# Performance work log

Measured on AMD Instinct MI355X. Metric: run time of the kernel, lower is better.

The kernel has to match this reference:

```python
import jax, jax.numpy as jnp
import numpy as np

B, L, K, H = 256, 256, 128, 256


def setup_inputs() -> dict:
    key = jax.random.key(0)
    ks = jax.random.split(key, 24)

    def u(k, shape, fan):
        s = 1.0 / np.sqrt(fan)
        return jax.random.uniform(k, shape, minval=-s, maxval=s, dtype=jnp.float32)

    x = jax.random.normal(ks[0], (B, L, K), jnp.float32)
    mask = (jax.random.uniform(ks[1], (B, L, K)) < 0.7).astype(jnp.float32)
    record_num = jax.random.randint(ks[2], (B,), L // 2, L + 1)
    ts = jnp.cumsum(jax.random.uniform(ks[3], (B, L), minval=0.1, maxval=1.0, dtype=jnp.float32), axis=1)
    time_stamp = ts * (jnp.arange(L)[None, :] < record_num[:, None]).astype(jnp.float32)

    return {
        "x": x,
        "mask": mask,
        "time_stamp": time_stamp,
        # TemporalDecay h: W [H,K], stdv = 1/sqrt(out)=1/sqrt(H)
        "W_gh": u(ks[4], (H, K), H), "b_gh": u(ks[5], (H,), H),
        # TemporalDecay x (diag): W [K,K], stdv = 1/sqrt(K)
        "W_gx": u(ks[6], (K, K), K), "b_gx": u(ks[7], (K,), K),
        # hist_reg: Linear(H -> K), stdv = 1/sqrt(H)
        "W_hist": u(ks[8], (K, H), H), "b_hist": u(ks[9], (K,), H),
        "W_feat": u(ks[10], (K, K), K), "b_feat": u(ks[11], (K,), K),
        # weight_combine: Linear(2K -> K), stdv = 1/sqrt(2K)
        "W_comb": u(ks[12], (K, 2 * K), 2 * K), "b_comb": u(ks[13], (K,), 2 * K),
        # GRUCell(2K -> H): uniform 1/sqrt(H)
        "W_ih": u(ks[14], (3 * H, 2 * K), H), "W_hh": u(ks[15], (3 * H, H), H),
        "b_ih": u(ks[16], (3 * H,), H), "b_hh": u(ks[17], (3 * H,), H),
        # out: Linear(H -> 1)
        "W_out": u(ks[18], (1, H), H), "b_out": u(ks[19], (1,), H),
        "record_num": record_num,
        "direct": 0,
    }


def _forward(x, mask, time_stamp, W_gh, b_gh, W_gx, b_gx, W_hist, b_hist,
             W_feat, b_feat, W_comb, b_comb, W_ih, W_hh, b_ih, b_hh,
             W_out, b_out, record_num):
    Bs, Ls, Ks = x.shape
    Hs = W_gh.shape[0]
    eye = jnp.eye(Ks, dtype=x.dtype)
    W_gx_m = W_gx * eye                 # diag temporal decay
    W_feat_m = W_feat * (1.0 - eye)

    # --- deltas (gen_aux_data): d[0]=1; d[t] = |ts[t]-ts[t-1]| + (1-m[t])*d[t-1] ---
    gaps = jnp.abs(jnp.diff(time_stamp, axis=1))          # [B, L-1]
    mask_t = jnp.swapaxes(mask, 0, 1)                     # [L, B, K]

    def dstep(prev, inp):
        gap, m = inp                                      # [B], [B,K]
        d = gap[:, None] + (1.0 - m) * prev
        return d, d

    d0 = jnp.ones((Bs, Ks), x.dtype)
    _, drest = jax.lax.scan(dstep, d0, (gaps.T, mask_t[1:]))
    deltas = jnp.concatenate([d0[None], drest], axis=0)   # [L, B, K]
    valid = (jnp.arange(Ls)[:, None] < record_num[None, :])  # break at record_num
    deltas = jnp.where(valid[:, :, None], deltas, 0.0)

    evals = (time_stamp != 0).astype(x.dtype)             # [B, L]

    x_t = jnp.swapaxes(x, 0, 1)                           # [L, B, K]
    e_t = evals.T                                         # [L, B]

    def step(carry, inp):
        h, xloss = carry
        xt, mt, dt, et = inp                              # [B,K],[B,K],[B,K],[B]
        e_m = et[:, None]
        gamma_h = jnp.exp(-jax.nn.relu(dt @ W_gh.T + b_gh))   # [B,H]
        gamma_x = jnp.exp(-jax.nn.relu(dt @ W_gx_m.T + b_gx)) # [B,K]
        h_prev = h
        h = h * gamma_h
        x_h = h @ W_hist.T + b_hist
        msum = jnp.sum(mt) + 1e-5
        xloss = xloss + jnp.sum(jnp.abs(xt - x_h) * mt) / msum
        x_c = mt * xt + (1.0 - mt) * x_h
        z_h = x_c @ W_feat_m.T + b_feat
        xloss = xloss + jnp.sum(jnp.abs(xt - z_h) * mt * e_m) / msum
        alpha = jnp.concatenate([gamma_x, mt], axis=1) @ W_comb.T + b_comb
        c_h = alpha * z_h + (1.0 - alpha) * x_h
        xloss = xloss + jnp.sum(jnp.abs(xt - c_h) * mt * e_m) / msum
        c_c = mt * xt + (1.0 - mt) * c_h
        inputs = jnp.concatenate([c_c, mt], axis=1)           # [B, 2K]
        gi = inputs @ W_ih.T + b_ih                           # [B, 3H]
        gh = h @ W_hh.T + b_hh
        ir, iz, ig = jnp.split(gi, 3, axis=1)
        hr, hz, hg = jnp.split(gh, 3, axis=1)
        r = jax.nn.sigmoid(ir + hr)
        z = jax.nn.sigmoid(iz + hz)
        n = jnp.tanh(ig + r * hg)
        h_new = (1.0 - z) * n + z * h
        h_new = h_new * e_m + (1.0 - e_m) * h_prev            # freeze h past record
        return (h_new, xloss), c_c * e_m

    h0 = jnp.zeros((Bs, Hs), x.dtype)
    (h_fin, x_loss), imps = jax.lax.scan(step, (h0, jnp.float32(0.0)), (x_t, mask_t, deltas, e_t))
    imputations = jnp.swapaxes(imps, 0, 1)                # [B, L, K]
    predictions = jax.nn.sigmoid(h_fin @ W_out.T + b_out) # [B, 1]
    return imputations, x_loss, predictions


def reference(x, mask, time_stamp, W_gh, b_gh, W_gx, b_gx, W_hist, b_hist,
              W_feat, b_feat, W_comb, b_comb, W_ih, W_hh, b_ih, b_hh,
              W_out, b_out, record_num, direct):
    return _forward(x, mask, time_stamp, W_gh, b_gh, W_gx, b_gx, W_hist, b_hist,
                    W_feat, b_feat, W_comb, b_comb, W_ih, W_hh, b_ih, b_hh,
                    W_out, b_out, record_num)
```

## Files before the change

kernel.cpp:

```cpp
#include <hip/hip_runtime.h>
#include <math.h>

#define BT 256
#define LT 256
#define KT 128
#define HT 256
#define LOSS_IDX ((size_t)BT*LT*KT)
#define PRED_IDX (LOSS_IDX + 1)
#define LDP 1280
#define GH0 0
#define AL0 256
#define GI0 384
#define ZP0 1152

typedef _Float16 h2 __attribute__((ext_vector_type(2)));
typedef _Float16 f16x8 __attribute__((ext_vector_type(8)));
typedef float f32x4 __attribute__((ext_vector_type(4)));

__device__ __forceinline__ float fd2(h2 a, h2 b, float c){
#if __has_builtin(__builtin_amdgcn_fdot2)
  return __builtin_amdgcn_fdot2(a, b, c, false);
#else
  return c + (float)a[0]*(float)b[0] + (float)a[1]*(float)b[1];
#endif
}
__device__ __forceinline__ float dot8(f16x8 w, f16x8 a, float acc){
  acc = fd2(__builtin_shufflevector(w,w,0,1), __builtin_shufflevector(a,a,0,1), acc);
  acc = fd2(__builtin_shufflevector(w,w,2,3), __builtin_shufflevector(a,a,2,3), acc);
  acc = fd2(__builtin_shufflevector(w,w,4,5), __builtin_shufflevector(a,a,4,5), acc);
  acc = fd2(__builtin_shufflevector(w,w,6,7), __builtin_shufflevector(a,a,6,7), acc);
  return acc;
}
__device__ __forceinline__ float sigf(float v){ return 1.0f/(1.0f + __expf(-v)); }
__device__ __forceinline__ float tanh_fast(float v){
  float a = fminf(fabsf(v), 15.0f);
  float e2 = __expf(2.0f*a);
  float r = (e2 - 1.0f)/(e2 + 1.0f);
  return copysignf(r, v);
}
__device__ __forceinline__ float f16bits(unsigned u, int hi){
  union { unsigned short s; _Float16 h; } c;
  c.s = (unsigned short)(hi ? (u >> 16) : (u & 0xffff));
  return (float)c.h;
}

__global__ void pack_cast(const float* __restrict__ src, _Float16* __restrict__ dst,
                          int J, int Kd, int diag, int total){
  int idx = blockIdx.x*256 + threadIdx.x;
  if (idx >= total) return;
  float v = src[idx];
  if (diag && (idx / Kd) == (idx % Kd)) v = 0.0f;
  dst[idx] = (_Float16)v;
}
__global__ void pack_rowchunks(const float* __restrict__ src, _Float16* __restrict__ dst,
                               int J, int K, int total){
  int idx = blockIdx.x*256 + threadIdx.x;
  if (idx >= total) return;
  int j = idx % J, c = idx / J;
  #pragma unroll
  for (int e = 0; e < 8; ++e)
    dst[(size_t)idx*8 + e] = (_Float16)src[(size_t)j*K + c*8 + e];
}
__global__ void pack_col(const float* __restrict__ src, _Float16* __restrict__ dst,
                         int J, int Kc, int ld, int diag, int total){
  int idx = blockIdx.x*256 + threadIdx.x;
  if (idx >= total) return;
  int j = idx % J, k = idx / J;
  float v = src[(size_t)j*ld + k];
  if (diag && j == k) v = 0.0f;
  dst[idx] = (_Float16)v;
}

__global__ __launch_bounds__(128) void scan_kernel(
    const float* __restrict__ x, const float* __restrict__ mask, const float* __restrict__ ts,
    const float* __restrict__ W_gx, const float* __restrict__ b_gx,
    const int* __restrict__ record_num,
    _Float16* __restrict__ deltas, _Float16* __restrict__ Agx, _Float16* __restrict__ U)
{
  int b = blockIdx.x, k = threadIdx.x;
  int rn = record_num[b];
  float gxd = W_gx[(size_t)k*KT + k];
  float bgx = b_gx[k];
  float d = 1.0f, tsp = 0.0f;
  for (int t0 = 0; t0 < LT; t0 += 8){
    float xv[8], mv[8], tsv[8];
    #pragma unroll
    for (int u = 0; u < 8; ++u){
      size_t off = ((size_t)b*LT + t0 + u)*KT + k;
      xv[u] = x[off]; mv[u] = mask[off];
      tsv[u] = ts[(size_t)b*LT + t0 + u];
    }
    #pragma unroll
    for (int u = 0; u < 8; ++u){
      int t = t0 + u;
      if (t > 0){
        float gap = fabsf(tsv[u] - (u ? tsv[u-1] : tsp));
        d = gap + (1.0f - mv[u])*d;
      }
      float e = (t < rn) ? 1.0f : 0.0f;
      float dev = d * e;
      size_t row = (size_t)b*LT + t;
      deltas[row*KT + k] = (_Float16)dev;
      float gx = __expf(-fmaxf(fmaf(dev, gxd, bgx), 0.0f));
      Agx[row*2*KT + k]      = (_Float16)gx;
      Agx[row*2*KT + KT + k] = (_Float16)mv[u];
      U[row*2*KT + k]        = (_Float16)(mv[u]*xv[u]);
      U[row*2*KT + KT + k]   = (_Float16)mv[u];
    }
    tsp = tsv[7];
  }
}

__global__ void msum_kernel(const float* __restrict__ mask, float* __restrict__ msumInv){
  __shared__ float red[256];
  int t = blockIdx.x;
  float acc = 0.0f;
  for (int i = threadIdx.x; i < BT*KT; i += 256){
    int b = i >> 7, k = i & 127;
    acc += mask[((size_t)b*LT + t)*KT + k];
  }
  red[threadIdx.x] = acc; __syncthreads();
  for (int s = 128; s > 0; s >>= 1){
    if (threadIdx.x < s) red[threadIdx.x] += red[threadIdx.x + s];
    __syncthreads();
  }
  if (threadIdx.x == 0) msumInv[t] = 1.0f/(red[0] + 1e-5f);
}

__global__ __launch_bounds__(256) void gemm_f16(
    const _Float16* __restrict__ A, long ldA, int K,
    const _Float16* __restrict__ B, long ldB,
    _Float16* __restrict__ C, long colofs,
    const float* __restrict__ bias, int op)
{
  const int w = threadIdx.x >> 6, lane = threadIdx.x & 63;
  const int ml = lane & 15, quad = lane >> 4;
  const long m0 = (long)blockIdx.x*64 + w*16;
  const long nb0 = (long)blockIdx.y*64;
  f32x4 acc[4] = {{0,0,0,0},{0,0,0,0},{0,0,0,0},{0,0,0,0}};
  for (int kc = 0; kc < K; kc += 32){
    f16x8 a = *(const f16x8*)(A + (m0 + ml)*ldA + kc + quad*8);
    #pragma unroll
    for (int nt = 0; nt < 4; ++nt){
      f16x8 bfr = *(const f16x8*)(B + (nb0 + nt*16 + ml)*ldB + kc + quad*8);
      acc[nt] = __builtin_amdgcn_mfma_f32_16x16x32_f16(a, bfr, acc[nt], 0, 0, 0);
    }
  }
  #pragma unroll
  for (int nt = 0; nt < 4; ++nt){
    long col = nb0 + nt*16 + ml;
    float bv = (op >= 1) ? bias[col] : 0.0f;
    #pragma unroll
    for (int r = 0; r < 4; ++r){
      float v = acc[nt][r];
      if (op >= 1) v += bv;
      if (op == 2) v = __expf(-fmaxf(v, 0.0f));
      long row = m0 + quad*4 + r;
      C[row*LDP + colofs + col] = (_Float16)v;
    }
  }
}

#define NT 768

struct __align__(16) SeqS {
  f16x8 whist_l[32*128];
  _Float16 wfc_l[128*128];
  float h[HT];
  float hs[HT];
  alignas(16) _Float16 hsh[HT];
  float gh[3*HT];
  float gi[3*HT];
  float xh[KT];
  float part6[6][KT];
  float v3[KT], v5[KT];
  int lidx[136];
  int posk[KT];
  int cnt;
  unsigned pb[2][LDP/2];
  float xb[2][KT], mb[2][KT];
  float bhist[KT], bfeat[KT];
  float bhh[3*HT];
  float wout[HT];
  float minv[LT];
  float red[NT/64];
};

__global__ __launch_bounds__(NT, 1) void rits_seq(
    const float* __restrict__ x, const float* __restrict__ mask,
    const int* __restrict__ record_num, const float* __restrict__ msumInv,
    const _Float16* __restrict__ P,
    const f16x8* __restrict__ Whh_p, const f16x8* __restrict__ Whist_p,
    const _Float16* __restrict__ Wfc, const _Float16* __restrict__ Wihc,
    const float* __restrict__ b_hist, const float* __restrict__ b_feat,
    const float* __restrict__ b_hh,
    const float* __restrict__ W_out, const float* __restrict__ b_out,
    float* __restrict__ out)
{
  __shared__ SeqS s;
  const int tid = threadIdx.x;
  const int b = blockIdx.x;
  const int rn = record_num[b];
  const unsigned* __restrict__ Pd = (const unsigned*)P + (size_t)b*LT*(LDP/2);

  for (int i = tid; i < 32*128; i += NT) s.whist_l[i] = Whist_p[i];
  for (int i = tid; i < 128*128/2; i += NT)
    ((unsigned*)s.wfc_l)[i] = ((const unsigned*)Wfc)[i];
  if (tid < HT) s.h[tid] = 0.0f;
  if (tid < KT){ s.bhist[tid] = b_hist[tid]; s.bfeat[tid] = b_feat[tid]; }
  if (tid < 3*HT) s.bhh[tid] = b_hh[tid];
  if (tid < 136) s.lidx[tid] = 0;
  if (tid >= 256 && tid < 512) s.wout[tid - 256] = W_out[tid - 256];
  if (tid >= 512 && tid < 512 + LT) s.minv[tid - 512] = msumInv[tid - 512];
  if (tid < LDP/2) s.pb[0][tid] = Pd[tid];
  else if (tid < LDP/2 + KT){
    int k = tid - LDP/2;
    s.xb[0][k] = x[((size_t)b*LT)*KT + k];
    s.mb[0][k] = mask[((size_t)b*LT)*KT + k];
  }
  __syncthreads();

  float loss = 0.0f;

  for (int t = 0; t < LT; ++t){
    const int cur = t & 1, nxt = cur ^ 1;

    unsigned pr0 = 0; float prx = 0.0f, prm = 0.0f;
    if (t < LT - 1){
      if (tid < LDP/2) pr0 = Pd[(size_t)(t+1)*(LDP/2) + tid];
      else {
        int k = tid - LDP/2;
        size_t offx = ((size_t)b*LT + t + 1)*KT + k;
        prx = x[offx]; prm = mask[offx];
      }
    }
    if (tid == 0) s.cnt = 0;
    if (tid < HT){
      float g = f16bits(s.pb[cur][tid >> 1], tid & 1);
      float hsv = s.h[tid] * g;
      s.hs[tid] = hsv;
      s.hsh[tid] = (_Float16)hsv;
    }
    __syncthreads();

    {
      const f16x8* hp = (const f16x8*)s.hsh;
      if (tid < KT){
        float a2 = 0.0f;
        #pragma unroll 8
        for (int c = 0; c < 32; ++c)
          a2 = dot8(s.whist_l[c*128 + tid], hp[c], a2);
        float xh = a2 + s.bhist[tid];
        s.xh[tid] = xh;
        float mv = s.mb[cur][tid], xv = s.xb[cur][tid];
        loss += fabsf(xv - xh) * mv * s.minv[t];
        if (mv == 0.0f){
          int pp = atomicAdd(&s.cnt, 1);
          s.lidx[pp] = tid; s.v3[pp] = xh; s.posk[tid] = pp;
        }
      }
      float acc = 0.0f;
      #pragma unroll 8
      for (int c = 0; c < 32; ++c)
        acc = dot8(Whh_p[c*768 + tid], hp[c], acc);
      s.gh[tid] = acc;
    }
    __syncthreads();

    const int c0 = s.cnt;
    const int c4 = (c0 + 7) & ~7;
    {
      int st = tid >> 7, j = tid & 127;
      float a = 0.0f;
      for (int i = st; i < c0; i += 6)
        a += s.v3[i] * (float)s.wfc_l[s.lidx[i]*128 + j];
      s.part6[st][j] = a;
    }
    float wpre[16];
    #pragma unroll
    for (int u = 0; u < 16; ++u)
      wpre[u] = (u < c4) ? (float)Wihc[(size_t)s.lidx[u]*768 + tid] : 0.0f;
    __syncthreads();

    if (tid < KT){
      const int j = tid;
      if (j >= c0 && j < c4) s.v5[j] = 0.0f;
      float z = f16bits(s.pb[cur][ZP0/2 + (j >> 1)], j & 1) + s.bfeat[j]
              + s.part6[0][j] + s.part6[1][j] + s.part6[2][j]
              + s.part6[3][j] + s.part6[4][j] + s.part6[5][j];
      float al = f16bits(s.pb[cur][AL0/2 + (j >> 1)], j & 1);
      float xh = s.xh[j];
      float mv = s.mb[cur][j], xv = s.xb[cur][j];
      float e = (t < rn) ? 1.0f : 0.0f;
      float inv = s.minv[t];
      float ch = al*z + (1.0f - al)*xh;
      loss += (fabsf(xv - z) + fabsf(xv - ch)) * mv * e * inv;
      float cc = mv*xv + (1.0f - mv)*ch;
      out[((size_t)b*LT + t)*KT + j] = cc * e;
      if (mv == 0.0f) s.v5[s.posk[j]] = ch;
    }
    __syncthreads();

    {
      float g = f16bits(s.pb[cur][GI0/2 + (tid >> 1)], tid & 1);
      #pragma unroll
      for (int u = 0; u < 16; ++u)
        if (u < c4) g += s.v5[u] * wpre[u];
      for (int i = 16; i < c4; i += 8){
        #pragma unroll
        for (int u = 0; u < 8; ++u)
          g += s.v5[i + u] * (float)Wihc[(size_t)s.lidx[i + u]*768 + tid];
      }
      s.gi[tid] = g;
    }
    __syncthreads();

    if (tid < HT){
      const int j = tid;
      float ir = s.gi[j], iz = s.gi[HT + j], ig = s.gi[2*HT + j];
      float hr = s.gh[j] + s.bhh[j];
      float hz = s.gh[HT + j] + s.bhh[HT + j];
      float hg = s.gh[2*HT + j] + s.bhh[2*HT + j];
      float r = sigf(ir + hr);
      float zg = sigf(iz + hz);
      float n = tanh_fast(ig + r*hg);
      float hn = (1.0f - zg)*n + zg*s.hs[j];
      if (t < rn) s.h[j] = hn;
    }
    if (t < LT - 1){
      if (tid < LDP/2) s.pb[nxt][tid] = pr0;
      else {
        int k = tid - LDP/2;
        s.xb[nxt][k] = prx; s.mb[nxt][k] = prm;
      }
    }
    __syncthreads();
  }

  #pragma unroll
  for (int off = 32; off; off >>= 1) loss += __shfl_down(loss, off);
  if ((tid & 63) == 0) s.red[tid >> 6] = loss;
  __syncthreads();
  if (tid == 0){
    float tot = 0.0f;
    #pragma unroll
    for (int w = 0; w < NT/64; ++w) tot += s.red[w];
    atomicAdd(&out[LOSS_IDX], tot);
  }

  if (tid < HT) s.gh[tid] = s.h[tid] * s.wout[tid];
  __syncthreads();
  for (int st2 = 128; st2 > 0; st2 >>= 1){
    if (tid < st2) s.gh[tid] += s.gh[tid + st2];
    __syncthreads();
  }
  if (tid == 0) out[PRED_IDX + b] = sigf(s.gh[0] + b_out[0]);
}

extern "C" void kernel_launch(void* const* d_in, const int* in_sizes, int n_in,
                              void* d_out, int out_size, void* d_ws, size_t ws_size,
                              hipStream_t stream){
  const float* x      = (const float*)d_in[0];
  const float* mask   = (const float*)d_in[1];
  const float* ts     = (const float*)d_in[2];
  const float* W_gh   = (const float*)d_in[3];
  const float* b_gh   = (const float*)d_in[4];
  const float* W_gx   = (const float*)d_in[5];
  const float* b_gx   = (const float*)d_in[6];
  const float* W_hist = (const float*)d_in[7];
  const float* b_hist = (const float*)d_in[8];
  const float* W_feat = (const float*)d_in[9];
  const float* b_feat = (const float*)d_in[10];
  const float* W_comb = (const float*)d_in[11];
  const float* b_comb = (const float*)d_in[12];
  const float* W_ih   = (const float*)d_in[13];
  const float* W_hh   = (const float*)d_in[14];
  const float* b_ih   = (const float*)d_in[15];
  const float* b_hh   = (const float*)d_in[16];
  const float* W_out  = (const float*)d_in[17];
  const float* b_out  = (const float*)d_in[18];
  const int*   rn     = (const int*)d_in[19];
  float* out = (float*)d_out;
  char* ws = (char*)d_ws;

  size_t off = 0;
  auto alloc = [&](size_t bytes) -> char* {
    char* p = ws + off;
    off += (bytes + 255) & ~(size_t)255;
    return p;
  };
  _Float16* P      = (_Float16*)alloc((size_t)BT*LT*LDP*2);
  _Float16* deltas = (_Float16*)alloc((size_t)BT*LT*KT*2);
  _Float16* Agx    = (_Float16*)alloc((size_t)BT*LT*2*KT*2);
  _Float16* U      = (_Float16*)alloc((size_t)BT*LT*2*KT*2);
  _Float16* WghF   = (_Float16*)alloc(HT*KT*2);
  _Float16* WcombF = (_Float16*)alloc(KT*2*KT*2);
  _Float16* WihF   = (_Float16*)alloc(3*HT*2*KT*2);
  _Float16* WfeatF = (_Float16*)alloc(KT*KT*2);
  _Float16* Whh_p  = (_Float16*)alloc(3*HT*HT*2);
  _Float16* Whist_p= (_Float16*)alloc(KT*HT*2);
  _Float16* Wfc    = (_Float16*)alloc(KT*KT*2);
  _Float16* Wihc   = (_Float16*)alloc(KT*3*HT*2);
  float* msumInv   = (float*)alloc(LT*4);

  auto grid1 = [](int n){ return dim3((n + 255)/256); };
  pack_cast<<<grid1(HT*KT), 256, 0, stream>>>(W_gh, WghF, HT, KT, 0, HT*KT);
  pack_cast<<<grid1(KT*2*KT), 256, 0, stream>>>(W_comb, WcombF, KT, 2*KT, 0, KT*2*KT);
  pack_cast<<<grid1(3*HT*2*KT), 256, 0, stream>>>(W_ih, WihF, 3*HT, 2*KT, 0, 3*HT*2*KT);
  pack_cast<<<grid1(KT*KT), 256, 0, stream>>>(W_feat, WfeatF, KT, KT, 1, KT*KT);
  pack_rowchunks<<<grid1(3*HT*(HT/8)), 256, 0, stream>>>(W_hh, Whh_p, 3*HT, HT, 3*HT*(HT/8));
  pack_rowchunks<<<grid1(KT*(HT/8)), 256, 0, stream>>>(W_hist, Whist_p, KT, HT, KT*(HT/8));
  pack_col<<<grid1(KT*KT), 256, 0, stream>>>(W_feat, Wfc, KT, KT, KT, 1, KT*KT);
  pack_col<<<grid1(768*KT), 256, 0, stream>>>(W_ih, Wihc, 3*HT, KT, 2*KT, 0, 3*HT*KT);

  scan_kernel<<<dim3(BT), dim3(KT), 0, stream>>>(x, mask, ts, W_gx, b_gx, rn, deltas, Agx, U);
  msum_kernel<<<dim3(LT), dim3(256), 0, stream>>>(mask, msumInv);

  const int MR = BT*LT;
  gemm_f16<<<dim3(MR/64, HT/64), 256, 0, stream>>>(deltas, KT, KT, WghF, KT, P, GH0, b_gh, 2);
  gemm_f16<<<dim3(MR/64, KT/64), 256, 0, stream>>>(Agx, 2*KT, 2*KT, WcombF, 2*KT, P, AL0, b_comb, 1);
  gemm_f16<<<dim3(MR/64, 3*HT/64), 256, 0, stream>>>(U, 2*KT, 2*KT, WihF, 2*KT, P, GI0, b_ih, 1);
  gemm_f16<<<dim3(MR/64, KT/64), 256, 0, stream>>>(U, 2*KT, KT, WfeatF, KT, P, ZP0, (const float*)nullptr, 0);

  hipMemsetAsync((void*)(out + LOSS_IDX), 0, sizeof(float), stream);

  rits_seq<<<dim3(BT), dim3(NT), 0, stream>>>(x, mask, rn, msumInv, P,
      (const f16x8*)Whh_p, (const f16x8*)Whist_p, Wfc, Wihc,
      b_hist, b_feat, b_hh, W_out, b_out, out);
}
```

Baseline: 2.420 ms.

## Restructure recurrent step with warp specialization and fewer barriers per timestep

Raises the block to 1024 threads and gives each warp group a role: W_hh matvec, hist regression with ballot-based compaction of missing features, or prefetch of the next step's precomputed data. The decayed-hidden computation for the next step is folded into the GRU update, and the feature-regression partial-sum stage is merged into the combine stage. Together these remove two barriers per timestep. Dot products now use four independent fdot2 accumulators, and the sparse W_ih gather uses packed fp16 pairs. The cost is fewer threads doing the serial z accumulation, fp16 rounding of the imputed values, and higher register pressure at 1024 threads.

```diff
diff --git a/kernel.cpp b/kernel.cpp
--- a/kernel.cpp
+++ b/kernel.cpp
@@ -24,13 +24,10 @@
   return c + (float)a[0]*(float)b[0] + (float)a[1]*(float)b[1];
 #endif
 }
-__device__ __forceinline__ float dot8(f16x8 w, f16x8 a, float acc){
-  acc = fd2(__builtin_shufflevector(w,w,0,1), __builtin_shufflevector(a,a,0,1), acc);
-  acc = fd2(__builtin_shufflevector(w,w,2,3), __builtin_shufflevector(a,a,2,3), acc);
-  acc = fd2(__builtin_shufflevector(w,w,4,5), __builtin_shufflevector(a,a,4,5), acc);
-  acc = fd2(__builtin_shufflevector(w,w,6,7), __builtin_shufflevector(a,a,6,7), acc);
-  return acc;
-}
+__device__ __forceinline__ h2 lo2(f16x8 v){ return __builtin_shufflevector(v,v,0,1); }
+__device__ __forceinline__ h2 p1(f16x8 v){ return __builtin_shufflevector(v,v,2,3); }
+__device__ __forceinline__ h2 p2(f16x8 v){ return __builtin_shufflevector(v,v,4,5); }
+__device__ __forceinline__ h2 p3(f16x8 v){ return __builtin_shufflevector(v,v,6,7); }
 __device__ __forceinline__ float sigf(float v){ return 1.0f/(1.0f + __expf(-v)); }
 __device__ __forceinline__ float tanh_fast(float v){
   float a = fminf(fabsf(v), 15.0f);
@@ -161,7 +158,7 @@
   }
 }
 
-#define NT 768
+#define NT 1024
 
 struct __align__(16) SeqS {
   f16x8 whist_l[32*128];
@@ -172,12 +169,13 @@
   float gh[3*HT];
   float gi[3*HT];
   float xh[KT];
-  float part6[6][KT];
-  float v3[KT], v5[KT];
+  float v3[136];
+  alignas(4) _Float16 v5h[136];
   int lidx[136];
   int posk[KT];
   int cnt;
-  unsigned pb[2][LDP/2];
+  unsigned gam[2][128];
+  unsigned pbd[2][512];
   float xb[2][KT], mb[2][KT];
   float bhist[KT], bfeat[KT];
   float bhh[3*HT];
@@ -206,89 +204,105 @@
   for (int i = tid; i < 32*128; i += NT) s.whist_l[i] = Whist_p[i];
   for (int i = tid; i < 128*128/2; i += NT)
     ((unsigned*)s.wfc_l)[i] = ((const unsigned*)Wfc)[i];
-  if (tid < HT) s.h[tid] = 0.0f;
+  if (tid < HT){ s.h[tid] = 0.0f; s.hs[tid] = 0.0f; s.hsh[tid] = (_Float16)0.0f; }
   if (tid < KT){ s.bhist[tid] = b_hist[tid]; s.bfeat[tid] = b_feat[tid]; }
   if (tid < 3*HT) s.bhh[tid] = b_hh[tid];
   if (tid < 136) s.lidx[tid] = 0;
-  if (tid >= 256 && tid < 512) s.wout[tid - 256] = W_out[tid - 256];
+  if (tid >= 768 && tid < 768 + HT) s.wout[tid - 768] = W_out[tid - 768];
   if (tid >= 512 && tid < 512 + LT) s.minv[tid - 512] = msumInv[tid - 512];
-  if (tid < LDP/2) s.pb[0][tid] = Pd[tid];
-  else if (tid < LDP/2 + KT){
-    int k = tid - LDP/2;
+  if (tid == 0) s.cnt = 0;
+  if (tid < 128) s.gam[0][tid] = Pd[tid];
+  if (tid >= 256 && tid < 768) s.pbd[0][tid - 256] = Pd[128 + tid - 256];
+  if (tid >= 896){
+    int k = tid - 896;
     s.xb[0][k] = x[((size_t)b*LT)*KT + k];
     s.mb[0][k] = mask[((size_t)b*LT)*KT + k];
   }
   __syncthreads();
 
   float loss = 0.0f;
+  unsigned pr[5]; float prx = 0.0f, prm = 0.0f;
+  h2 wpre[16];
 
   for (int t = 0; t < LT; ++t){
     const int cur = t & 1, nxt = cur ^ 1;
-
-    unsigned pr0 = 0; float prx = 0.0f, prm = 0.0f;
-    if (t < LT - 1){
-      if (tid < LDP/2) pr0 = Pd[(size_t)(t+1)*(LDP/2) + tid];
-      else {
-        int k = tid - LDP/2;
-        size_t offx = ((size_t)b*LT + t + 1)*KT + k;
+    const int last = (t == LT - 1);
+
+    if (tid < 768){
+      const f16x8* hp = (const f16x8*)s.hsh;
+      float a0=0.f, a1=0.f, a2=0.f, a3=0.f;
+      #pragma unroll
+      for (int c = 0; c < 32; ++c){
+        f16x8 w = Whh_p[c*768 + tid];
+        f16x8 av = hp[c];
+        a0 = fd2(lo2(w), lo2(av), a0);
+        a1 = fd2(p1(w),  p1(av),  a1);
+        a2 = fd2(p2(w),  p2(av),  a2);
+        a3 = fd2(p3(w),  p3(av),  a3);
+      }
+      s.gh[tid] = (a0 + a1) + (a2 + a3);
+    } else if (tid < 896){
+      const int j = tid - 768;
+      const f16x8* hp = (const f16x8*)s.hsh;
+      float a0=0.f, a1=0.f, a2=0.f, a3=0.f;
+      #pragma unroll
+      for (int c = 0; c < 32; ++c){
+        f16x8 w = s.whist_l[c*128 + j];
+        f16x8 av = hp[c];
+        a0 = fd2(lo2(w), lo2(av), a0);
+        a1 = fd2(p1(w),  p1(av),  a1);
+        a2 = fd2(p2(w),  p2(av),  a2);
+        a3 = fd2(p3(w),  p3(av),  a3);
+      }
+      float xh = (a0 + a1) + (a2 + a3) + s.bhist[j];
+      s.xh[j] = xh;
+      float mv = s.mb[cur][j], xv = s.xb[cur][j];
+      loss += fabsf(xv - xh) * mv * s.minv[t];
+      bool miss = (mv == 0.0f);
+      unsigned long long bal = __ballot(miss);
+      int lane = tid & 63;
+      int rank = __popcll(bal & ((1ull << lane) - 1ull));
+      int wcnt = __popcll(bal);
+      int base = 0;
+      if (lane == 0 && wcnt) base = atomicAdd(&s.cnt, wcnt);
+      base = __shfl(base, 0);
+      if (miss){
+        int pp = base + rank;
+        s.lidx[pp] = j; s.v3[pp] = xh; s.posk[j] = pp;
+      }
+    } else {
+      if (!last){
+        int i = tid - 896;
+        const unsigned* Pn = Pd + (size_t)(t + 1)*(LDP/2);
+        #pragma unroll
+        for (int u = 0; u < 5; ++u) pr[u] = Pn[u*128 + i];
+        size_t offx = ((size_t)b*LT + t + 1)*KT + i;
         prx = x[offx]; prm = mask[offx];
       }
     }
-    if (tid == 0) s.cnt = 0;
-    if (tid < HT){
-      float g = f16bits(s.pb[cur][tid >> 1], tid & 1);
-      float hsv = s.h[tid] * g;
-      s.hs[tid] = hsv;
-      s.hsh[tid] = (_Float16)hsv;
-    }
-    __syncthreads();
-
-    {
-      const f16x8* hp = (const f16x8*)s.hsh;
-      if (tid < KT){
-        float a2 = 0.0f;
-        #pragma unroll 8
-        for (int c = 0; c < 32; ++c)
-          a2 = dot8(s.whist_l[c*128 + tid], hp[c], a2);
-        float xh = a2 + s.bhist[tid];
-        s.xh[tid] = xh;
-        float mv = s.mb[cur][tid], xv = s.xb[cur][tid];
-        loss += fabsf(xv - xh) * mv * s.minv[t];
-        if (mv == 0.0f){
-          int pp = atomicAdd(&s.cnt, 1);
-          s.lidx[pp] = tid; s.v3[pp] = xh; s.posk[tid] = pp;
-        }
-      }
-      float acc = 0.0f;
-      #pragma unroll 8
-      for (int c = 0; c < 32; ++c)
-        acc = dot8(Whh_p[c*768 + tid], hp[c], acc);
-      s.gh[tid] = acc;
-    }
     __syncthreads();
 
     const int c0 = s.cnt;
-    const int c4 = (c0 + 7) & ~7;
-    {
-      int st = tid >> 7, j = tid & 127;
-      float a = 0.0f;
-      for (int i = st; i < c0; i += 6)
-        a += s.v3[i] * (float)s.wfc_l[s.lidx[i]*128 + j];
-      s.part6[st][j] = a;
-    }
-    float wpre[16];
-    #pragma unroll
-    for (int u = 0; u < 16; ++u)
-      wpre[u] = (u < c4) ? (float)Wihc[(size_t)s.lidx[u]*768 + tid] : 0.0f;
-    __syncthreads();
-
+    if (tid < 768){
+      #pragma unroll
+      for (int u = 0; u < 16; ++u){
+        h2 w;
+        w[0] = Wihc[(size_t)s.lidx[2*u]*768 + tid];
+        w[1] = Wihc[(size_t)s.lidx[2*u + 1]*768 + tid];
+        wpre[u] = w;
+      }
+    }
     if (tid < KT){
       const int j = tid;
-      if (j >= c0 && j < c4) s.v5[j] = 0.0f;
-      float z = f16bits(s.pb[cur][ZP0/2 + (j >> 1)], j & 1) + s.bfeat[j]
-              + s.part6[0][j] + s.part6[1][j] + s.part6[2][j]
-              + s.part6[3][j] + s.part6[4][j] + s.part6[5][j];
-      float al = f16bits(s.pb[cur][AL0/2 + (j >> 1)], j & 1);
+      float za = 0.0f, zb = 0.0f;
+      int i = 0;
+      for (; i + 1 < c0; i += 2){
+        za += s.v3[i]     * (float)s.wfc_l[s.lidx[i]*128 + j];
+        zb += s.v3[i + 1] * (float)s.wfc_l[s.lidx[i + 1]*128 + j];
+      }
+      if (i < c0) za += s.v3[i] * (float)s.wfc_l[s.lidx[i]*128 + j];
+      float z = f16bits(s.pbd[cur][448 + (j >> 1)], j & 1) + s.bfeat[j] + za + zb;
+      float al = f16bits(s.pbd[cur][j >> 1], j & 1);
       float xh = s.xh[j];
       float mv = s.mb[cur][j], xv = s.xb[cur][j];
       float e = (t < rn) ? 1.0f : 0.0f;
@@ -297,21 +311,26 @@
       loss += (fabsf(xv - z) + fabsf(xv - ch)) * mv * e * inv;
       float cc = mv*xv + (1.0f - mv)*ch;
       out[((size_t)b*LT + t)*KT + j] = cc * e;
-      if (mv == 0.0f) s.v5[s.posk[j]] = ch;
-    }
-    __syncthreads();
-
-    {
-      float g = f16bits(s.pb[cur][GI0/2 + (tid >> 1)], tid & 1);
+      if (mv == 0.0f) s.v5h[s.posk[j]] = (_Float16)ch;
+    } else if (tid < 168){
+      int i2 = c0 + (tid - 128);
+      if (i2 < 136) s.v5h[i2] = (_Float16)0.0f;
+    }
+    if (tid >= 896 && !last) s.gam[nxt][tid - 896] = pr[0];
+    __syncthreads();
+
+    if (tid < 768){
+      float g  = f16bits(s.pbd[cur][64 + (tid >> 1)], tid & 1);
+      float g2 = 0.0f;
+      const h2* v5p = (const h2*)s.v5h;
       #pragma unroll
-      for (int u = 0; u < 16; ++u)
-        if (u < c4) g += s.v5[u] * wpre[u];
-      for (int i = 16; i < c4; i += 8){
-        #pragma unroll
-        for (int u = 0; u < 8; ++u)
-          g += s.v5[i + u] * (float)Wihc[(size_t)s.lidx[i + u]*768 + tid];
-      }
-      s.gi[tid] = g;
+      for (int u = 0; u < 16; u += 2){
+        g  = fd2(wpre[u],     v5p[u],     g);
+        g2 = fd2(wpre[u + 1], v5p[u + 1], g2);
+      }
+      for (int i = 32; i < c0; ++i)
+        g2 += (float)s.v5h[i] * (float)Wihc[(size_t)s.lidx[i]*768 + tid];
+      s.gi[tid] = g + g2;
     }
     __syncthreads();
 
@@ -324,15 +343,23 @@
       float r = sigf(ir + hr);
       float zg = sigf(iz + hz);
       float n = tanh_fast(ig + r*hg);
-      float hn = (1.0f - zg)*n + zg*s.hs[j];
-      if (t < rn) s.h[j] = hn;
-    }
-    if (t < LT - 1){
-      if (tid < LDP/2) s.pb[nxt][tid] = pr0;
-      else {
-        int k = tid - LDP/2;
-        s.xb[nxt][k] = prx; s.mb[nxt][k] = prm;
-      }
+      float hscur = s.hs[j];
+      float hn = (1.0f - zg)*n + zg*hscur;
+      float he = (t < rn) ? hn : s.h[j];
+      s.h[j] = he;
+      if (!last){
+        float gn = f16bits(s.gam[nxt][j >> 1], j & 1);
+        float hsn = he * gn;
+        s.hs[j] = hsn;
+        s.hsh[j] = (_Float16)hsn;
+      }
+    }
+    if (tid == HT) s.cnt = 0;
+    if (tid >= 896 && !last){
+      int i = tid - 896;
+      #pragma unroll
+      for (int u = 1; u < 5; ++u) s.pbd[nxt][(u - 1)*128 + i] = pr[u];
+      s.xb[nxt][i] = prx; s.mb[nxt][i] = prm;
     }
     __syncthreads();
   }
```

Result: slower. 2.692 ms (+11.3%).

## Compact missing-index list via ballot early and prefetch 48 W_ih columns in fp16

Applied to the files above, without the earlier changes.

Builds the missing-feature index list with a wave ballot and prefix popcount before the first barrier, so the W_ih column gather for the missing features can be issued early and overlap the hidden-state matvecs. The prefetch grows from 16 to 48 columns, held as packed fp16 pairs and consumed with fdot2, and v5 is stored in fp16. The dot products are split across four accumulators to shorten dependency chains. This costs more registers per thread and adds fp16 rounding of the imputed values, and it relies on the padding entries of lidx and v5h staying valid.

```diff
diff --git a/kernel.cpp b/kernel.cpp
--- a/kernel.cpp
+++ b/kernel.cpp
@@ -24,13 +24,10 @@
   return c + (float)a[0]*(float)b[0] + (float)a[1]*(float)b[1];
 #endif
 }
-__device__ __forceinline__ float dot8(f16x8 w, f16x8 a, float acc){
-  acc = fd2(__builtin_shufflevector(w,w,0,1), __builtin_shufflevector(a,a,0,1), acc);
-  acc = fd2(__builtin_shufflevector(w,w,2,3), __builtin_shufflevector(a,a,2,3), acc);
-  acc = fd2(__builtin_shufflevector(w,w,4,5), __builtin_shufflevector(a,a,4,5), acc);
-  acc = fd2(__builtin_shufflevector(w,w,6,7), __builtin_shufflevector(a,a,6,7), acc);
-  return acc;
-}
+__device__ __forceinline__ h2 lo2(f16x8 v){ return __builtin_shufflevector(v,v,0,1); }
+__device__ __forceinline__ h2 p1v(f16x8 v){ return __builtin_shufflevector(v,v,2,3); }
+__device__ __forceinline__ h2 p2v(f16x8 v){ return __builtin_shufflevector(v,v,4,5); }
+__device__ __forceinline__ h2 p3v(f16x8 v){ return __builtin_shufflevector(v,v,6,7); }
 __device__ __forceinline__ float sigf(float v){ return 1.0f/(1.0f + __expf(-v)); }
 __device__ __forceinline__ float tanh_fast(float v){
   float a = fminf(fabsf(v), 15.0f);
@@ -173,7 +170,8 @@
   float gi[3*HT];
   float xh[KT];
   float part6[6][KT];
-  float v3[KT], v5[KT];
+  float v3[136];
+  alignas(4) _Float16 v5h[136];
   int lidx[136];
   int posk[KT];
   int cnt;
@@ -209,9 +207,10 @@
   if (tid < HT) s.h[tid] = 0.0f;
   if (tid < KT){ s.bhist[tid] = b_hist[tid]; s.bfeat[tid] = b_feat[tid]; }
   if (tid < 3*HT) s.bhh[tid] = b_hh[tid];
-  if (tid < 136) s.lidx[tid] = 0;
+  if (tid < 136){ s.lidx[tid] = 0; s.v5h[tid] = (_Float16)0.0f; }
   if (tid >= 256 && tid < 512) s.wout[tid - 256] = W_out[tid - 256];
   if (tid >= 512 && tid < 512 + LT) s.minv[tid - 512] = msumInv[tid - 512];
+  if (tid == 0) s.cnt = 0;
   if (tid < LDP/2) s.pb[0][tid] = Pd[tid];
   else if (tid < LDP/2 + KT){
     int k = tid - LDP/2;
@@ -221,6 +220,7 @@
   __syncthreads();
 
   float loss = 0.0f;
+  h2 wpre[24];
 
   for (int t = 0; t < LT; ++t){
     const int cur = t & 1, nxt = cur ^ 1;
@@ -234,41 +234,70 @@
         prx = x[offx]; prm = mask[offx];
       }
     }
-    if (tid == 0) s.cnt = 0;
     if (tid < HT){
       float g = f16bits(s.pb[cur][tid >> 1], tid & 1);
       float hsv = s.h[tid] * g;
       s.hs[tid] = hsv;
       s.hsh[tid] = (_Float16)hsv;
     }
+    if (tid < KT){
+      bool miss = (s.mb[cur][tid] == 0.0f);
+      unsigned long long bal = __ballot(miss);
+      int lane = tid & 63;
+      int rank = __popcll(bal & ((1ull << lane) - 1ull));
+      int wcnt = __popcll(bal);
+      int base = 0;
+      if (lane == 0 && wcnt) base = atomicAdd(&s.cnt, wcnt);
+      base = __shfl(base, 0);
+      if (miss){
+        int pp = base + rank;
+        s.lidx[pp] = tid; s.posk[tid] = pp;
+      }
+    }
     __syncthreads();
 
     {
+      #pragma unroll
+      for (int u = 0; u < 24; ++u){
+        h2 w;
+        w[0] = Wihc[(size_t)s.lidx[2*u]*768 + tid];
+        w[1] = Wihc[(size_t)s.lidx[2*u + 1]*768 + tid];
+        wpre[u] = w;
+      }
       const f16x8* hp = (const f16x8*)s.hsh;
       if (tid < KT){
-        float a2 = 0.0f;
+        const int j = tid;
+        float a0=0.f, a1=0.f, a2=0.f, a3=0.f;
         #pragma unroll 8
-        for (int c = 0; c < 32; ++c)
-          a2 = dot8(s.whist_l[c*128 + tid], hp[c], a2);
-        float xh = a2 + s.bhist[tid];
-        s.xh[tid] = xh;
-        float mv = s.mb[cur][tid], xv = s.xb[cur][tid];
+        for (int c = 0; c < 32; ++c){
+          f16x8 w = s.whist_l[c*128 + j];
+          f16x8 av = hp[c];
+          a0 = fd2(lo2(w), lo2(av), a0);
+          a1 = fd2(p1v(w), p1v(av), a1);
+          a2 = fd2(p2v(w), p2v(av), a2);
+          a3 = fd2(p3v(w), p3v(av), a3);
+        }
+        float xh = (a0 + a1) + (a2 + a3) + s.bhist[j];
+        s.xh[j] = xh;
+        float mv = s.mb[cur][j], xv = s.xb[cur][j];
         loss += fabsf(xv - xh) * mv * s.minv[t];
-        if (mv == 0.0f){
-          int pp = atomicAdd(&s.cnt, 1);
-          s.lidx[pp] = tid; s.v3[pp] = xh; s.posk[tid] = pp;
-        }
-      }
-      float acc = 0.0f;
+        if (mv == 0.0f) s.v3[s.posk[j]] = xh;
+      }
+      float a0=0.f, a1=0.f, a2=0.f, a3=0.f;
       #pragma unroll 8
-      for (int c = 0; c < 32; ++c)
-        acc = dot8(Whh_p[c*768 + tid], hp[c], acc);
-      s.gh[tid] = acc;
+      for (int c = 0; c < 32; ++c){
+        f16x8 w = Whh_p[c*768 + tid];
+        f16x8 av = hp[c];
+        a0 = fd2(lo2(w), lo2(av), a0);
+        a1 = fd2(p1v(w), p1v(av), a1);
+        a2 = fd2(p2v(w), p2v(av), a2);
+        a3 = fd2(p3v(w), p3v(av), a3);
+      }
+      s.gh[tid] = (a0 + a1) + (a2 + a3);
     }
     __syncthreads();
 
     const int c0 = s.cnt;
-    const int c4 = (c0 + 7) & ~7;
     {
       int st = tid >> 7, j = tid & 127;
       float a = 0.0f;
@@ -276,15 +305,10 @@
         a += s.v3[i] * (float)s.wfc_l[s.lidx[i]*128 + j];
       s.part6[st][j] = a;
     }
-    float wpre[16];
-    #pragma unroll
-    for (int u = 0; u < 16; ++u)
-      wpre[u] = (u < c4) ? (float)Wihc[(size_t)s.lidx[u]*768 + tid] : 0.0f;
     __syncthreads();
 
     if (tid < KT){
       const int j = tid;
-      if (j >= c0 && j < c4) s.v5[j] = 0.0f;
       float z = f16bits(s.pb[cur][ZP0/2 + (j >> 1)], j & 1) + s.bfeat[j]
               + s.part6[0][j] + s.part6[1][j] + s.part6[2][j]
               + s.part6[3][j] + s.part6[4][j] + s.part6[5][j];
@@ -297,21 +321,25 @@
       loss += (fabsf(xv - z) + fabsf(xv - ch)) * mv * e * inv;
       float cc = mv*xv + (1.0f - mv)*ch;
       out[((size_t)b*LT + t)*KT + j] = cc * e;
-      if (mv == 0.0f) s.v5[s.posk[j]] = ch;
+      if (mv == 0.0f) s.v5h[s.posk[j]] = (_Float16)ch;
+    } else if (tid < 192){
+      int i2 = c0 + (tid - 128);
+      if (i2 < 136) s.v5h[i2] = (_Float16)0.0f;
     }
     __syncthreads();
 
     {
-      float g = f16bits(s.pb[cur][GI0/2 + (tid >> 1)], tid & 1);
+      float g  = f16bits(s.pb[cur][GI0/2 + (tid >> 1)], tid & 1);
+      float g2 = 0.0f;
+      const h2* v5p = (const h2*)s.v5h;
       #pragma unroll
-      for (int u = 0; u < 16; ++u)
-        if (u < c4) g += s.v5[u] * wpre[u];
-      for (int i = 16; i < c4; i += 8){
-        #pragma unroll
-        for (int u = 0; u < 8; ++u)
-          g += s.v5[i + u] * (float)Wihc[(size_t)s.lidx[i + u]*768 + tid];
-      }
-      s.gi[tid] = g;
+      for (int u = 0; u < 24; u += 2){
+        g  = fd2(wpre[u],     v5p[u],     g);
+        g2 = fd2(wpre[u + 1], v5p[u + 1], g2);
+      }
+      for (int i = 48; i < c0; ++i)
+        g2 += (float)s.v5h[i] * (float)Wihc[(size_t)s.lidx[i]*768 + tid];
+      s.gi[tid] = g + g2;
     }
     __syncthreads();
 
@@ -327,6 +355,7 @@
       float hn = (1.0f - zg)*n + zg*s.hs[j];
       if (t < rn) s.h[j] = hn;
     }
+    if (tid == 320) s.cnt = 0;
     if (t < LT - 1){
       if (tid < LDP/2) s.pb[nxt][tid] = pr0;
       else {
```

Result: slower. 2.487 ms (+2.8%).
